# Performance work log

Hardware: AMD Instinct MI355X
Metric: run time of the kernel (lower is better)

## Reference

```python
import jax, jax.numpy as jnp
import numpy as np

H = 16
QK_DIM = 1024
EPS = 1e-5


def setup_inputs() -> dict:
    key = jax.random.key(0)
    ks = jax.random.split(key, 5)
    B, N, M, D = 2, 2048, 2048, 1024
    x = jax.random.normal(ks[0], (B, N, D), jnp.float32)
    context = jax.random.normal(ks[1], (B, M, D), jnp.float32)
    Wq = jax.random.normal(ks[2], (QK_DIM, D), jnp.float32) * (D ** -0.5)
    Wkv = jax.random.normal(ks[3], (QK_DIM + 1024, D), jnp.float32) * (D ** -0.5)
    Wtalk = jax.random.normal(ks[4], (H, H), jnp.float32) * (H ** -0.5)
    ln_gamma = jnp.ones((H,), jnp.float32)
    ln_beta = jnp.zeros((H,), jnp.float32)
    return {"x": x, "context": context, "Wq": Wq, "Wkv": Wkv,
            "Wtalk": Wtalk, "ln_gamma": ln_gamma, "ln_beta": ln_beta}


def _split_heads(t):
    # b n (h d) -> b h n d
    b, n, hd = t.shape
    return t.reshape(b, n, H, hd // H).transpose(0, 2, 1, 3)


def reference(x, context, Wq, Wkv, Wtalk, ln_gamma, ln_beta):
    q = x @ Wq.T                      # [B,N,QK]
    kv = context @ Wkv.T              # [B,M,QK+V]
    k, v = kv[..., :QK_DIM], kv[..., QK_DIM:]
    q, k, v = _split_heads(q), _split_heads(k), _split_heads(v)
    q = q * (q.shape[-1] ** -0.5)
    scores = jnp.einsum('bhid,bhjd->bhij', q, k)          # [B,H,N,M]
    aw = jax.nn.softmax(scores, axis=-1)
    # talking heads: Linear over head axis then LayerNorm over head axis
    aw = jnp.einsum('bhij,gh->bgij', aw, Wtalk)
    mu = jnp.mean(aw, axis=1, keepdims=True)
    var = jnp.var(aw, axis=1, keepdims=True)
    aw = (aw - mu) * jax.lax.rsqrt(var + EPS)
    aw = aw * ln_gamma[None, :, None, None] + ln_beta[None, :, None, None]
    attn = jnp.einsum('bhij,bhjd->bhid', aw, v)           # [B,H,N,dv]
    b, h, n, d = attn.shape
    return attn.transpose(0, 2, 1, 3).reshape(b, n, h * d)  # [B,N,V]
```

## Files before the change

### kernel.cpp

```cpp
#include <hip/hip_runtime.h>


typedef __attribute__((ext_vector_type(8))) short short8;
typedef __attribute__((ext_vector_type(4))) short short4v;
typedef __attribute__((ext_vector_type(4))) float float4v;
typedef unsigned short u16;

#define MFMA16(a, b, c) __builtin_amdgcn_mfma_f32_16x16x32_bf16((a), (b), (c), 0, 0, 0)

__device__ inline u16 f2bf(float f) {
  unsigned u = __float_as_uint(f);
  u += 0x7FFFu + ((u >> 16) & 1u);
  return (u16)(u >> 16);
}

__global__ __launch_bounds__(256) void cast_bf16(const float* __restrict__ in,
                                                 u16* __restrict__ out, int n) {
  int i = (blockIdx.x * 256 + threadIdx.x) * 8;
  if (i + 8 > n) return;
  float4v f0 = *(const float4v*)(in + i);
  float4v f1 = *(const float4v*)(in + i + 4);
  short8 o;
  o[0] = (short)f2bf(f0[0]); o[1] = (short)f2bf(f0[1]);
  o[2] = (short)f2bf(f0[2]); o[3] = (short)f2bf(f0[3]);
  o[4] = (short)f2bf(f1[0]); o[5] = (short)f2bf(f1[1]);
  o[6] = (short)f2bf(f1[2]); o[7] = (short)f2bf(f1[3]);
  *(short8*)(out + i) = o;
}

template <int MODE>
__global__ __launch_bounds__(256, 4) void gemm_bt(const u16* __restrict__ A,
                                                  const u16* __restrict__ W,
                                                  u16* __restrict__ out0,
                                                  u16* __restrict__ out1) {
  __shared__ u16 As[64][40];
  __shared__ u16 Ws[64][40];
  const int t = threadIdx.x;
  const int wave = t >> 6, l = t & 63, l15 = l & 15, lq = l >> 4;
  const int r0 = blockIdx.x * 64, c0 = blockIdx.y * 64;
  const int srow = t >> 2, sch = t & 3;
  const u16* ag = A + (r0 + srow) * 1024 + sch * 8;
  const u16* wg = W + (c0 + srow) * 1024 + sch * 8;

  float4v acc[4];
#pragma unroll
  for (int i = 0; i < 4; ++i) acc[i] = (float4v){0.f, 0.f, 0.f, 0.f};

  short8 av = *(const short8*)ag;
  short8 wv = *(const short8*)wg;
  for (int kt = 0; kt < 32; ++kt) {
    __syncthreads();
    *(short8*)&As[srow][sch * 8] = av;
    *(short8*)&Ws[srow][sch * 8] = wv;
    __syncthreads();
    if (kt < 31) {
      av = *(const short8*)(ag + (kt + 1) * 32);
      wv = *(const short8*)(wg + (kt + 1) * 32);
    }
    short8 af = *(const short8*)&As[wave * 16 + l15][lq * 8];
#pragma unroll
    for (int fn = 0; fn < 4; ++fn) {
      short8 bf = *(const short8*)&Ws[fn * 16 + l15][lq * 8];
      acc[fn] = MFMA16(af, bf, acc[fn]);
    }
  }
#pragma unroll
  for (int fn = 0; fn < 4; ++fn) {
#pragma unroll
    for (int r = 0; r < 4; ++r) {
      int row = r0 + wave * 16 + lq * 4 + r;
      int col = c0 + fn * 16 + l15;
      int b = row >> 11, n = row & 2047;
      float v = acc[fn][r];
      if (MODE == 0) {
        v *= 0.125f;
        int h = col >> 6, d = col & 63;
        out0[(((b * 16 + h) * 2048 + n) << 6) + d] = f2bf(v);
      } else {
        if (col < 1024) {
          int h = col >> 6, d = col & 63;
          out0[(((b * 16 + h) * 2048 + n) << 6) + d] = f2bf(v);
        } else {
          int cc = col - 1024;
          int h = cc >> 6, d = cc & 63;
          out1[(((b * 16 + h) * 2048 + n) << 6) + d] = f2bf(v);
        }
      }
    }
  }
}

__global__ __launch_bounds__(256) void transpose_v(const u16* __restrict__ vh,
                                                   u16* __restrict__ vt) {
  __shared__ u16 tile[64][72];
  const int t = threadIdx.x;
  const int j0 = blockIdx.x * 64, h = blockIdx.y, b = blockIdx.z;
  const u16* src = vh + (((b * 16 + h) * 2048 + j0) << 6);
  int row = t >> 2, c = t & 3;
  short8 v0 = *(const short8*)(src + row * 64 + c * 8);
  short8 v1 = *(const short8*)(src + row * 64 + (c + 4) * 8);
  *(short8*)&tile[row][c * 8] = v0;
  *(short8*)&tile[row][(c + 4) * 8] = v1;
  __syncthreads();
  int d = t >> 2, jc = t & 3;
  short8 o0, o1;
#pragma unroll
  for (int jj = 0; jj < 8; ++jj) o0[jj] = (short)tile[jc * 16 + jj][d];
#pragma unroll
  for (int jj = 0; jj < 8; ++jj) o1[jj] = (short)tile[jc * 16 + 8 + jj][d];
  u16* dst = vt + ((b * 16 + h) * 64 + d) * 2048 + j0 + jc * 16;
  *(short8*)dst = o0;
  *(short8*)(dst + 8) = o1;
}

__global__ __launch_bounds__(1024) void attn_fused(
    const u16* __restrict__ qh, const u16* __restrict__ kh,
    const u16* __restrict__ vt, const float* __restrict__ wtalk,
    const float* __restrict__ gamma, const float* __restrict__ beta,
    float* __restrict__ out) {
  __shared__ u16 P_lds[512 * 36];
  __shared__ u16 Y_lds[16 * 16 * 32];

  const int tid = threadIdx.x;
  const int wv = tid >> 6;
  const int l = tid & 63, l15 = l & 15, lq = l >> 4;
  const int bid = blockIdx.x;
  const int b = bid & 1;
  const int i0 = (bid >> 1) * 16;

  for (int z = tid; z < 512 * 36; z += 1024) P_lds[z] = 0;

  short8 wfrag;
#pragma unroll
  for (int t8 = 0; t8 < 8; ++t8) {
    int h = lq * 8 + t8;
    float wval = (h < 16) ? wtalk[l15 * 16 + h] : 0.f;
    wfrag[t8] = (short)f2bf(wval);
  }
  float gam[4], bet[4];
#pragma unroll
  for (int r = 0; r < 4; ++r) {
    gam[r] = gamma[lq * 4 + r];
    bet[r] = beta[lq * 4 + r];
  }

  const u16* qbase = qh + (((b * 16 + wv) * 2048 + i0) << 6);
  short8 qf0 = *(const short8*)(qbase + l15 * 64 + lq * 8);
  short8 qf1 = *(const short8*)(qbase + l15 * 64 + 32 + lq * 8);
  const u16* kbase = kh + (((b * 16 + wv) * 2048) << 6);
  const u16* vbase = vt + ((b * 16 + wv) * 64) * 2048;

  __syncthreads();

  float ps0 = 0.f, ps1 = 0.f, ps2 = 0.f, ps3 = 0.f;
  short8 k00 = *(const short8*)(kbase + l15 * 64 + lq * 8);
  short8 k01 = *(const short8*)(kbase + l15 * 64 + 32 + lq * 8);
  short8 k10 = *(const short8*)(kbase + (16 + l15) * 64 + lq * 8);
  short8 k11 = *(const short8*)(kbase + (16 + l15) * 64 + 32 + lq * 8);
  for (int jt = 0; jt < 64; ++jt) {
    short8 n00, n01, n10, n11;
    if (jt < 63) {
      const u16* kp = kbase + (((jt + 1) * 32) << 6);
      n00 = *(const short8*)(kp + l15 * 64 + lq * 8);
      n01 = *(const short8*)(kp + l15 * 64 + 32 + lq * 8);
      n10 = *(const short8*)(kp + (16 + l15) * 64 + lq * 8);
      n11 = *(const short8*)(kp + (16 + l15) * 64 + 32 + lq * 8);
    }
    float4v s0 = {0.f, 0.f, 0.f, 0.f}, s1 = {0.f, 0.f, 0.f, 0.f};
    s0 = MFMA16(qf0, k00, s0);
    s0 = MFMA16(qf1, k01, s0);
    s1 = MFMA16(qf0, k10, s1);
    s1 = MFMA16(qf1, k11, s1);
    ps0 += __expf(s0[0]) + __expf(s1[0]);
    ps1 += __expf(s0[1]) + __expf(s1[1]);
    ps2 += __expf(s0[2]) + __expf(s1[2]);
    ps3 += __expf(s0[3]) + __expf(s1[3]);
    k00 = n00; k01 = n01; k10 = n10; k11 = n11;
  }
#pragma unroll
  for (int d = 1; d < 16; d <<= 1) {
    ps0 += __shfl_xor(ps0, d);
    ps1 += __shfl_xor(ps1, d);
    ps2 += __shfl_xor(ps2, d);
    ps3 += __shfl_xor(ps3, d);
  }
  float bc[4];
  bc[0] = -logf(ps0); bc[1] = -logf(ps1);
  bc[2] = -logf(ps2); bc[3] = -logf(ps3);

  float4v acc0 = {0.f, 0.f, 0.f, 0.f}, acc1 = acc0, acc2 = acc0, acc3 = acc0;
  for (int jt = 0; jt < 64; ++jt) {
    const int j0 = jt * 32;
    const u16* kp = kbase + (j0 << 6);
    short8 a00 = *(const short8*)(kp + l15 * 64 + lq * 8);
    short8 a01 = *(const short8*)(kp + l15 * 64 + 32 + lq * 8);
    short8 a10 = *(const short8*)(kp + (16 + l15) * 64 + lq * 8);
    short8 a11 = *(const short8*)(kp + (16 + l15) * 64 + 32 + lq * 8);
    float4v s0 = {0.f, 0.f, 0.f, 0.f}, s1 = {0.f, 0.f, 0.f, 0.f};
    s0 = MFMA16(qf0, a00, s0);
    s0 = MFMA16(qf1, a01, s0);
    s1 = MFMA16(qf0, a10, s1);
    s1 = MFMA16(qf1, a11, s1);
    {
      int ebase = (lq * 4) * 32 + l15;
#pragma unroll
      for (int r = 0; r < 4; ++r) {
        float p0 = __expf(s0[r] + bc[r]);
        float p1 = __expf(s1[r] + bc[r]);
        P_lds[(ebase + r * 32) * 36 + wv] = f2bf(p0);
        P_lds[(ebase + r * 32 + 16) * 36 + wv] = f2bf(p1);
      }
    }
    __syncthreads();
    const u16* vp = vbase + j0 + lq * 8;
    short8 v0 = *(const short8*)(vp + (l15) * 2048);
    short8 v1 = *(const short8*)(vp + (16 + l15) * 2048);
    short8 v2 = *(const short8*)(vp + (32 + l15) * 2048);
    short8 v3 = *(const short8*)(vp + (48 + l15) * 2048);
    float4v t0 = {0.f, 0.f, 0.f, 0.f}, t1 = {0.f, 0.f, 0.f, 0.f};
    {
      int e00 = wv * 32 + l15;
      int e10 = wv * 32 + 16 + l15;
      const u16* p0p = &P_lds[e00 * 36 + lq * 8];
      const u16* p1p = &P_lds[e10 * 36 + lq * 8];
      short4v x0 = *(const short4v*)p0p;
      short4v x1 = *(const short4v*)(p0p + 4);
      short4v y0 = *(const short4v*)p1p;
      short4v y1 = *(const short4v*)(p1p + 4);
      short8 pb0 = __builtin_shufflevector(x0, x1, 0, 1, 2, 3, 4, 5, 6, 7);
      short8 pb1 = __builtin_shufflevector(y0, y1, 0, 1, 2, 3, 4, 5, 6, 7);
      t0 = MFMA16(wfrag, pb0, t0);
      t1 = MFMA16(wfrag, pb1, t1);
    }
#pragma unroll
    for (int c2 = 0; c2 < 2; ++c2) {
      float4v tt = c2 ? t1 : t0;
      float sum = tt[0] + tt[1] + tt[2] + tt[3];
      sum += __shfl_xor(sum, 16);
      sum += __shfl_xor(sum, 32);
      float mu = sum * 0.0625f;
      float ss = tt[0] * tt[0] + tt[1] * tt[1] + tt[2] * tt[2] + tt[3] * tt[3];
      ss += __shfl_xor(ss, 16);
      ss += __shfl_xor(ss, 32);
      float var = ss * 0.0625f - mu * mu;
      float rs = rsqrtf(var + 1e-5f);
#pragma unroll
      for (int r = 0; r < 4; ++r) {
        float y = (tt[r] - mu) * rs * gam[r] + bet[r];
        Y_lds[((lq * 4 + r) * 16 + wv) * 32 + c2 * 16 + l15] = f2bf(y);
      }
    }
    __syncthreads();
    short8 yf = *(const short8*)&Y_lds[(wv * 16 + l15) * 32 + lq * 8];
    acc0 = MFMA16(yf, v0, acc0);
    acc1 = MFMA16(yf, v1, acc1);
    acc2 = MFMA16(yf, v2, acc2);
    acc3 = MFMA16(yf, v3, acc3);
  }
  float* ob = out + (b * 2048 + i0) * 1024 + wv * 64;
#pragma unroll
  for (int r = 0; r < 4; ++r) {
    float* orow = ob + (lq * 4 + r) * 1024;
    orow[l15] = acc0[r];
    orow[16 + l15] = acc1[r];
    orow[32 + l15] = acc2[r];
    orow[48 + l15] = acc3[r];
  }
}

extern "C" void kernel_launch(void* const* d_in, const int* in_sizes, int n_in,
                              void* d_out, int out_size, void* d_ws,
                              size_t ws_size, hipStream_t stream) {
  const float* x = (const float*)d_in[0];
  const float* ctx = (const float*)d_in[1];
  const float* Wq = (const float*)d_in[2];
  const float* Wkv = (const float*)d_in[3];
  const float* Wtalk = (const float*)d_in[4];
  const float* gam = (const float*)d_in[5];
  const float* bet = (const float*)d_in[6];
  float* out = (float*)d_out;

  u16* xb = (u16*)d_ws;
  u16* cb = xb + 4194304;
  u16* wqb = cb + 4194304;
  u16* wkvb = wqb + 1048576;
  u16* qhb = wkvb + 2097152;
  u16* khb = qhb + 4194304;
  u16* vhb = khb + 4194304;
  u16* vtb = vhb + 4194304;

  cast_bf16<<<2048, 256, 0, stream>>>(x, xb, 4194304);
  cast_bf16<<<2048, 256, 0, stream>>>(ctx, cb, 4194304);
  cast_bf16<<<512, 256, 0, stream>>>(Wq, wqb, 1048576);
  cast_bf16<<<1024, 256, 0, stream>>>(Wkv, wkvb, 2097152);

  gemm_bt<0><<<dim3(64, 16), 256, 0, stream>>>(xb, wqb, qhb, nullptr);
  gemm_bt<1><<<dim3(64, 32), 256, 0, stream>>>(cb, wkvb, khb, vhb);

  transpose_v<<<dim3(32, 16, 2), 256, 0, stream>>>(vhb, vtb);

  attn_fused<<<256, 1024, 0, stream>>>(qhb, khb, vtb, Wtalk, gam, bet, out);
}
```

Baseline: 523.4 us.

## Split softmax denominator into separate kernel and split-K attention over key chunks

The softmax log-denominator pass moves out of the fused attention kernel into its own kernel, which writes per-row negative log-sums to workspace. The main attention kernel then splits the key dimension into 8 chunks across a 3D grid and accumulates partial outputs into a zeroed output buffer with atomic adds. This raises block count from 256 to 2048 so the GPU is better occupied, at the cost of a memset, an extra launch, and atomic traffic on the output.

```diff
diff --git a/kernel.cpp b/kernel.cpp
--- a/kernel.cpp
+++ b/kernel.cpp
@@ -113,44 +113,16 @@
   *(short8*)(dst + 8) = o1;
 }
 
-__global__ __launch_bounds__(1024) void attn_fused(
-    const u16* __restrict__ qh, const u16* __restrict__ kh,
-    const u16* __restrict__ vt, const float* __restrict__ wtalk,
-    const float* __restrict__ gamma, const float* __restrict__ beta,
-    float* __restrict__ out) {
-  __shared__ u16 P_lds[512 * 36];
-  __shared__ u16 Y_lds[16 * 16 * 32];
-
-  const int tid = threadIdx.x;
-  const int wv = tid >> 6;
-  const int l = tid & 63, l15 = l & 15, lq = l >> 4;
-  const int bid = blockIdx.x;
-  const int b = bid & 1;
-  const int i0 = (bid >> 1) * 16;
-
-  for (int z = tid; z < 512 * 36; z += 1024) P_lds[z] = 0;
-
-  short8 wfrag;
-#pragma unroll
-  for (int t8 = 0; t8 < 8; ++t8) {
-    int h = lq * 8 + t8;
-    float wval = (h < 16) ? wtalk[l15 * 16 + h] : 0.f;
-    wfrag[t8] = (short)f2bf(wval);
-  }
-  float gam[4], bet[4];
-#pragma unroll
-  for (int r = 0; r < 4; ++r) {
-    gam[r] = gamma[lq * 4 + r];
-    bet[r] = beta[lq * 4 + r];
-  }
-
-  const u16* qbase = qh + (((b * 16 + wv) * 2048 + i0) << 6);
+__global__ __launch_bounds__(256) void denom_kernel(const u16* __restrict__ qh,
+                                                    const u16* __restrict__ kh,
+                                                    float* __restrict__ negl) {
+  const int bh = blockIdx.x;
+  const int i0 = blockIdx.y * 64 + (threadIdx.x >> 6) * 16;
+  const int l = threadIdx.x & 63, l15 = l & 15, lq = l >> 4;
+  const u16* qbase = qh + ((bh * 2048 + i0) << 6);
   short8 qf0 = *(const short8*)(qbase + l15 * 64 + lq * 8);
   short8 qf1 = *(const short8*)(qbase + l15 * 64 + 32 + lq * 8);
-  const u16* kbase = kh + (((b * 16 + wv) * 2048) << 6);
-  const u16* vbase = vt + ((b * 16 + wv) * 64) * 2048;
-
-  __syncthreads();
+  const u16* kbase = kh + ((bh * 2048) << 6);
 
   float ps0 = 0.f, ps1 = 0.f, ps2 = 0.f, ps3 = 0.f;
   short8 k00 = *(const short8*)(kbase + l15 * 64 + lq * 8);
@@ -184,13 +156,59 @@
     ps2 += __shfl_xor(ps2, d);
     ps3 += __shfl_xor(ps3, d);
   }
-  float bc[4];
-  bc[0] = -logf(ps0); bc[1] = -logf(ps1);
-  bc[2] = -logf(ps2); bc[3] = -logf(ps3);
+  if (l15 == 0) {
+    float* o = negl + bh * 2048 + i0 + lq * 4;
+    o[0] = -logf(ps0);
+    o[1] = -logf(ps1);
+    o[2] = -logf(ps2);
+    o[3] = -logf(ps3);
+  }
+}
+
+__global__ __launch_bounds__(1024) void attn_fused(
+    const u16* __restrict__ qh, const u16* __restrict__ kh,
+    const u16* __restrict__ vt, const float* __restrict__ negl,
+    const float* __restrict__ wtalk, const float* __restrict__ gamma,
+    const float* __restrict__ beta, float* __restrict__ out) {
+  __shared__ u16 P_lds[512 * 36];
+  __shared__ u16 Y_lds[16 * 16 * 32];
+
+  const int tid = threadIdx.x;
+  const int wv = tid >> 6;
+  const int l = tid & 63, l15 = l & 15, lq = l >> 4;
+  const int i0 = blockIdx.x * 16;
+  const int jc0 = blockIdx.y * 256;
+  const int b = blockIdx.z;
+  const int bh = b * 16 + wv;
+
+  for (int z = tid; z < 512 * 36; z += 1024) P_lds[z] = 0;
+
+  short8 wfrag;
+#pragma unroll
+  for (int t8 = 0; t8 < 8; ++t8) {
+    int h = lq * 8 + t8;
+    float wval = (h < 16) ? wtalk[l15 * 16 + h] : 0.f;
+    wfrag[t8] = (short)f2bf(wval);
+  }
+  float gam[4], bet[4], bc[4];
+#pragma unroll
+  for (int r = 0; r < 4; ++r) {
+    gam[r] = gamma[lq * 4 + r];
+    bet[r] = beta[lq * 4 + r];
+    bc[r] = negl[bh * 2048 + i0 + lq * 4 + r];
+  }
+
+  const u16* qbase = qh + ((bh * 2048 + i0) << 6);
+  short8 qf0 = *(const short8*)(qbase + l15 * 64 + lq * 8);
+  short8 qf1 = *(const short8*)(qbase + l15 * 64 + 32 + lq * 8);
+  const u16* kbase = kh + ((bh * 2048) << 6);
+  const u16* vbase = vt + (bh * 64) * 2048;
+
+  __syncthreads();
 
   float4v acc0 = {0.f, 0.f, 0.f, 0.f}, acc1 = acc0, acc2 = acc0, acc3 = acc0;
-  for (int jt = 0; jt < 64; ++jt) {
-    const int j0 = jt * 32;
+  for (int jt = 0; jt < 8; ++jt) {
+    const int j0 = jc0 + jt * 32;
     const u16* kp = kbase + (j0 << 6);
     short8 a00 = *(const short8*)(kp + l15 * 64 + lq * 8);
     short8 a01 = *(const short8*)(kp + l15 * 64 + 32 + lq * 8);
@@ -261,10 +279,10 @@
 #pragma unroll
   for (int r = 0; r < 4; ++r) {
     float* orow = ob + (lq * 4 + r) * 1024;
-    orow[l15] = acc0[r];
-    orow[16 + l15] = acc1[r];
-    orow[32 + l15] = acc2[r];
-    orow[48 + l15] = acc3[r];
+    unsafeAtomicAdd(orow + l15, acc0[r]);
+    unsafeAtomicAdd(orow + 16 + l15, acc1[r]);
+    unsafeAtomicAdd(orow + 32 + l15, acc2[r]);
+    unsafeAtomicAdd(orow + 48 + l15, acc3[r]);
   }
 }
 
@@ -288,6 +306,9 @@
   u16* khb = qhb + 4194304;
   u16* vhb = khb + 4194304;
   u16* vtb = vhb + 4194304;
+  float* negl = (float*)(vtb + 4194304);
+
+  hipMemsetAsync(out, 0, 2 * 2048 * 1024 * sizeof(float), stream);
 
   cast_bf16<<<2048, 256, 0, stream>>>(x, xb, 4194304);
   cast_bf16<<<2048, 256, 0, stream>>>(ctx, cb, 4194304);
@@ -299,5 +320,8 @@
 
   transpose_v<<<dim3(32, 16, 2), 256, 0, stream>>>(vhb, vtb);
 
-  attn_fused<<<256, 1024, 0, stream>>>(qhb, khb, vtb, Wtalk, gam, bet, out);
-}
+  denom_kernel<<<dim3(32, 32), 256, 0, stream>>>(qhb, khb, negl);
+
+  attn_fused<<<dim3(128, 8, 2), 1024, 0, stream>>>(qhb, khb, vtb, negl, Wtalk,
+                                                   gam, bet, out);
+}
```

New measurement: 612.4 us. 1.17x slower.

## Double-buffer P and Y tiles to drop one barrier per iteration in attention

Applied to the files above, without the earlier changes.

The attention loop is software-pipelined. P and Y shared-memory tiles are double-buffered, K fragments for the next tile are prefetched, V loads are issued early, and the Y·V MFMA is deferred by one iteration, so each iteration needs one __syncthreads instead of two. Y_lds rows are padded from 32 to 36 to reduce bank conflicts. The grid becomes 2D so that consecutive blocks share the same batch, which may improve cache reuse of K and V. In exchange it doubles LDS use and raises register pressure. The padded 16-byte Y reads are no longer 16-byte aligned, which is a correctness and performance risk.

```diff
diff --git a/kernel.cpp b/kernel.cpp
--- a/kernel.cpp
+++ b/kernel.cpp
@@ -118,17 +118,20 @@
     const u16* __restrict__ vt, const float* __restrict__ wtalk,
     const float* __restrict__ gamma, const float* __restrict__ beta,
     float* __restrict__ out) {
-  __shared__ u16 P_lds[512 * 36];
-  __shared__ u16 Y_lds[16 * 16 * 32];
+  __shared__ u16 P_lds[2][512 * 36];
+  __shared__ u16 Y_lds[2][16 * 16 * 36];
 
   const int tid = threadIdx.x;
   const int wv = tid >> 6;
   const int l = tid & 63, l15 = l & 15, lq = l >> 4;
-  const int bid = blockIdx.x;
-  const int b = bid & 1;
-  const int i0 = (bid >> 1) * 16;
-
-  for (int z = tid; z < 512 * 36; z += 1024) P_lds[z] = 0;
+  const int i0 = blockIdx.x * 16;
+  const int b = blockIdx.y;
+  const int bh = b * 16 + wv;
+
+  {
+    u16* pz = &P_lds[0][0];
+    for (int z = tid; z < 2 * 512 * 36; z += 1024) pz[z] = 0;
+  }
 
   short8 wfrag;
 #pragma unroll
@@ -144,11 +147,11 @@
     bet[r] = beta[lq * 4 + r];
   }
 
-  const u16* qbase = qh + (((b * 16 + wv) * 2048 + i0) << 6);
+  const u16* qbase = qh + ((bh * 2048 + i0) << 6);
   short8 qf0 = *(const short8*)(qbase + l15 * 64 + lq * 8);
   short8 qf1 = *(const short8*)(qbase + l15 * 64 + 32 + lq * 8);
-  const u16* kbase = kh + (((b * 16 + wv) * 2048) << 6);
-  const u16* vbase = vt + ((b * 16 + wv) * 64) * 2048;
+  const u16* kbase = kh + ((bh * 2048) << 6);
+  const u16* vbase = vt + (bh * 64) * 2048;
 
   __syncthreads();
 
@@ -189,73 +192,88 @@
   bc[2] = -logf(ps2); bc[3] = -logf(ps3);
 
   float4v acc0 = {0.f, 0.f, 0.f, 0.f}, acc1 = acc0, acc2 = acc0, acc3 = acc0;
-  for (int jt = 0; jt < 64; ++jt) {
-    const int j0 = jt * 32;
-    const u16* kp = kbase + (j0 << 6);
-    short8 a00 = *(const short8*)(kp + l15 * 64 + lq * 8);
-    short8 a01 = *(const short8*)(kp + l15 * 64 + 32 + lq * 8);
-    short8 a10 = *(const short8*)(kp + (16 + l15) * 64 + lq * 8);
-    short8 a11 = *(const short8*)(kp + (16 + l15) * 64 + 32 + lq * 8);
-    float4v s0 = {0.f, 0.f, 0.f, 0.f}, s1 = {0.f, 0.f, 0.f, 0.f};
-    s0 = MFMA16(qf0, a00, s0);
-    s0 = MFMA16(qf1, a01, s0);
-    s1 = MFMA16(qf0, a10, s1);
-    s1 = MFMA16(qf1, a11, s1);
-    {
+  short8 kc00 = *(const short8*)(kbase + l15 * 64 + lq * 8);
+  short8 kc01 = *(const short8*)(kbase + l15 * 64 + 32 + lq * 8);
+  short8 kc10 = *(const short8*)(kbase + (16 + l15) * 64 + lq * 8);
+  short8 kc11 = *(const short8*)(kbase + (16 + l15) * 64 + 32 + lq * 8);
+  short8 v0, v1, v2, v3;
+
+  for (int jt = 0; jt <= 64; ++jt) {
+    const int buf = jt & 1, pbuf = (jt - 1) & 1;
+    if (jt >= 1) {
+      const u16* vp = vbase + (jt - 1) * 32 + lq * 8;
+      v0 = *(const short8*)(vp + (l15) * 2048);
+      v1 = *(const short8*)(vp + (16 + l15) * 2048);
+      v2 = *(const short8*)(vp + (32 + l15) * 2048);
+      v3 = *(const short8*)(vp + (48 + l15) * 2048);
+    }
+    short8 kn00, kn01, kn10, kn11;
+    if (jt + 1 < 64) {
+      const u16* kp = kbase + (((jt + 1) * 32) << 6);
+      kn00 = *(const short8*)(kp + l15 * 64 + lq * 8);
+      kn01 = *(const short8*)(kp + l15 * 64 + 32 + lq * 8);
+      kn10 = *(const short8*)(kp + (16 + l15) * 64 + lq * 8);
+      kn11 = *(const short8*)(kp + (16 + l15) * 64 + 32 + lq * 8);
+    }
+    if (jt < 64) {
+      float4v s0 = {0.f, 0.f, 0.f, 0.f}, s1 = {0.f, 0.f, 0.f, 0.f};
+      s0 = MFMA16(qf0, kc00, s0);
+      s0 = MFMA16(qf1, kc01, s0);
+      s1 = MFMA16(qf0, kc10, s1);
+      s1 = MFMA16(qf1, kc11, s1);
       int ebase = (lq * 4) * 32 + l15;
 #pragma unroll
       for (int r = 0; r < 4; ++r) {
         float p0 = __expf(s0[r] + bc[r]);
         float p1 = __expf(s1[r] + bc[r]);
-        P_lds[(ebase + r * 32) * 36 + wv] = f2bf(p0);
-        P_lds[(ebase + r * 32 + 16) * 36 + wv] = f2bf(p1);
+        P_lds[buf][(ebase + r * 32) * 36 + wv] = f2bf(p0);
+        P_lds[buf][(ebase + r * 32 + 16) * 36 + wv] = f2bf(p1);
       }
     }
     __syncthreads();
-    const u16* vp = vbase + j0 + lq * 8;
-    short8 v0 = *(const short8*)(vp + (l15) * 2048);
-    short8 v1 = *(const short8*)(vp + (16 + l15) * 2048);
-    short8 v2 = *(const short8*)(vp + (32 + l15) * 2048);
-    short8 v3 = *(const short8*)(vp + (48 + l15) * 2048);
-    float4v t0 = {0.f, 0.f, 0.f, 0.f}, t1 = {0.f, 0.f, 0.f, 0.f};
-    {
-      int e00 = wv * 32 + l15;
-      int e10 = wv * 32 + 16 + l15;
-      const u16* p0p = &P_lds[e00 * 36 + lq * 8];
-      const u16* p1p = &P_lds[e10 * 36 + lq * 8];
-      short4v x0 = *(const short4v*)p0p;
-      short4v x1 = *(const short4v*)(p0p + 4);
-      short4v y0 = *(const short4v*)p1p;
-      short4v y1 = *(const short4v*)(p1p + 4);
-      short8 pb0 = __builtin_shufflevector(x0, x1, 0, 1, 2, 3, 4, 5, 6, 7);
-      short8 pb1 = __builtin_shufflevector(y0, y1, 0, 1, 2, 3, 4, 5, 6, 7);
-      t0 = MFMA16(wfrag, pb0, t0);
-      t1 = MFMA16(wfrag, pb1, t1);
-    }
-#pragma unroll
-    for (int c2 = 0; c2 < 2; ++c2) {
-      float4v tt = c2 ? t1 : t0;
-      float sum = tt[0] + tt[1] + tt[2] + tt[3];
-      sum += __shfl_xor(sum, 16);
-      sum += __shfl_xor(sum, 32);
-      float mu = sum * 0.0625f;
-      float ss = tt[0] * tt[0] + tt[1] * tt[1] + tt[2] * tt[2] + tt[3] * tt[3];
-      ss += __shfl_xor(ss, 16);
-      ss += __shfl_xor(ss, 32);
-      float var = ss * 0.0625f - mu * mu;
-      float rs = rsqrtf(var + 1e-5f);
-#pragma unroll
-      for (int r = 0; r < 4; ++r) {
-        float y = (tt[r] - mu) * rs * gam[r] + bet[r];
-        Y_lds[((lq * 4 + r) * 16 + wv) * 32 + c2 * 16 + l15] = f2bf(y);
+    if (jt < 64) {
+      float4v t0 = {0.f, 0.f, 0.f, 0.f}, t1 = {0.f, 0.f, 0.f, 0.f};
+      {
+        int e00 = wv * 32 + l15;
+        int e10 = wv * 32 + 16 + l15;
+        const u16* p0p = &P_lds[buf][e00 * 36 + lq * 8];
+        const u16* p1p = &P_lds[buf][e10 * 36 + lq * 8];
+        short4v x0 = *(const short4v*)p0p;
+        short4v x1 = *(const short4v*)(p0p + 4);
+        short4v y0 = *(const short4v*)p1p;
+        short4v y1 = *(const short4v*)(p1p + 4);
+        short8 pb0 = __builtin_shufflevector(x0, x1, 0, 1, 2, 3, 4, 5, 6, 7);
+        short8 pb1 = __builtin_shufflevector(y0, y1, 0, 1, 2, 3, 4, 5, 6, 7);
+        t0 = MFMA16(wfrag, pb0, t0);
+        t1 = MFMA16(wfrag, pb1, t1);
       }
-    }
-    __syncthreads();
-    short8 yf = *(const short8*)&Y_lds[(wv * 16 + l15) * 32 + lq * 8];
-    acc0 = MFMA16(yf, v0, acc0);
-    acc1 = MFMA16(yf, v1, acc1);
-    acc2 = MFMA16(yf, v2, acc2);
-    acc3 = MFMA16(yf, v3, acc3);
+#pragma unroll
+      for (int c2 = 0; c2 < 2; ++c2) {
+        float4v tt = c2 ? t1 : t0;
+        float sum = tt[0] + tt[1] + tt[2] + tt[3];
+        sum += __shfl_xor(sum, 16);
+        sum += __shfl_xor(sum, 32);
+        float mu = sum * 0.0625f;
+        float ss = tt[0] * tt[0] + tt[1] * tt[1] + tt[2] * tt[2] + tt[3] * tt[3];
+        ss += __shfl_xor(ss, 16);
+        ss += __shfl_xor(ss, 32);
+        float var = ss * 0.0625f - mu * mu;
+        float rs = rsqrtf(var + 1e-5f);
+#pragma unroll
+        for (int r = 0; r < 4; ++r) {
+          float y = (tt[r] - mu) * rs * gam[r] + bet[r];
+          Y_lds[buf][((lq * 4 + r) * 16 + wv) * 36 + c2 * 16 + l15] = f2bf(y);
+        }
+      }
+    }
+    if (jt >= 1) {
+      short8 yf = *(const short8*)&Y_lds[pbuf][(wv * 16 + l15) * 36 + lq * 8];
+      acc0 = MFMA16(yf, v0, acc0);
+      acc1 = MFMA16(yf, v1, acc1);
+      acc2 = MFMA16(yf, v2, acc2);
+      acc3 = MFMA16(yf, v3, acc3);
+    }
+    kc00 = kn00; kc01 = kn01; kc10 = kn10; kc11 = kn11;
   }
   float* ob = out + (b * 2048 + i0) * 1024 + wv * 64;
 #pragma unroll
@@ -299,5 +317,6 @@
 
   transpose_v<<<dim3(32, 16, 2), 256, 0, stream>>>(vhb, vtb);
 
-  attn_fused<<<256, 1024, 0, stream>>>(qhb, khb, vtb, Wtalk, gam, bet, out);
-}
+  attn_fused<<<dim3(128, 2), 1024, 0, stream>>>(qhb, khb, vtb, Wtalk, gam, bet,
+                                                out);
+}
```

After: 506.7 us. -3.2%, faster.

## Split attention into denominator and split-key PV kernels with atomic accumulation

Applied to the files above, without the earlier changes.

Replaces the single fused attention kernel, which ran 256 blocks of 1024 threads, with two kernels. A separate denominator kernel computes the softmax sums over key chunks and accumulates them with atomics. A split-key PV kernel then runs 1024 blocks of 256 threads, where each wave handles 4 heads, and atomically adds partial outputs into a zeroed output buffer. The aim is more parallelism and better occupancy across CUs. The cost is extra memsets, float atomics on the full output, and a second pass recomputing QK scores.

```diff
diff --git a/kernel.cpp b/kernel.cpp
--- a/kernel.cpp
+++ b/kernel.cpp
@@ -5,6 +5,7 @@
 typedef __attribute__((ext_vector_type(4))) short short4v;
 typedef __attribute__((ext_vector_type(4))) float float4v;
 typedef unsigned short u16;
+typedef unsigned int u32;
 
 #define MFMA16(a, b, c) __builtin_amdgcn_mfma_f32_16x16x32_bf16((a), (b), (c), 0, 0, 0)
 
@@ -113,53 +114,27 @@
   *(short8*)(dst + 8) = o1;
 }
 
-__global__ __launch_bounds__(1024) void attn_fused(
-    const u16* __restrict__ qh, const u16* __restrict__ kh,
-    const u16* __restrict__ vt, const float* __restrict__ wtalk,
-    const float* __restrict__ gamma, const float* __restrict__ beta,
-    float* __restrict__ out) {
-  __shared__ u16 P_lds[512 * 36];
-  __shared__ u16 Y_lds[16 * 16 * 32];
-
-  const int tid = threadIdx.x;
-  const int wv = tid >> 6;
-  const int l = tid & 63, l15 = l & 15, lq = l >> 4;
+__global__ __launch_bounds__(256) void denom_kernel(const u16* __restrict__ qh,
+                                                    const u16* __restrict__ kh,
+                                                    float* __restrict__ lsum) {
   const int bid = blockIdx.x;
-  const int b = bid & 1;
-  const int i0 = (bid >> 1) * 16;
-
-  for (int z = tid; z < 512 * 36; z += 1024) P_lds[z] = 0;
-
-  short8 wfrag;
-#pragma unroll
-  for (int t8 = 0; t8 < 8; ++t8) {
-    int h = lq * 8 + t8;
-    float wval = (h < 16) ? wtalk[l15 * 16 + h] : 0.f;
-    wfrag[t8] = (short)f2bf(wval);
-  }
-  float gam[4], bet[4];
-#pragma unroll
-  for (int r = 0; r < 4; ++r) {
-    gam[r] = gamma[lq * 4 + r];
-    bet[r] = beta[lq * 4 + r];
-  }
-
-  const u16* qbase = qh + (((b * 16 + wv) * 2048 + i0) << 6);
+  const int bh = bid & 31, it = (bid >> 5) & 31, jc = bid >> 10;
+  const int wv = threadIdx.x >> 6;
+  const int i0 = it * 64 + wv * 16;
+  const int l = threadIdx.x & 63, l15 = l & 15, lq = l >> 4;
+  const u16* qbase = qh + ((bh * 2048 + i0) << 6);
   short8 qf0 = *(const short8*)(qbase + l15 * 64 + lq * 8);
   short8 qf1 = *(const short8*)(qbase + l15 * 64 + 32 + lq * 8);
-  const u16* kbase = kh + (((b * 16 + wv) * 2048) << 6);
-  const u16* vbase = vt + ((b * 16 + wv) * 64) * 2048;
-
-  __syncthreads();
+  const u16* kbase = kh + ((bh * 2048 + jc * 512) << 6);
 
   float ps0 = 0.f, ps1 = 0.f, ps2 = 0.f, ps3 = 0.f;
   short8 k00 = *(const short8*)(kbase + l15 * 64 + lq * 8);
   short8 k01 = *(const short8*)(kbase + l15 * 64 + 32 + lq * 8);
   short8 k10 = *(const short8*)(kbase + (16 + l15) * 64 + lq * 8);
   short8 k11 = *(const short8*)(kbase + (16 + l15) * 64 + 32 + lq * 8);
-  for (int jt = 0; jt < 64; ++jt) {
+  for (int jt = 0; jt < 16; ++jt) {
     short8 n00, n01, n10, n11;
-    if (jt < 63) {
+    if (jt < 15) {
       const u16* kp = kbase + (((jt + 1) * 32) << 6);
       n00 = *(const short8*)(kp + l15 * 64 + lq * 8);
       n01 = *(const short8*)(kp + l15 * 64 + 32 + lq * 8);
@@ -184,88 +159,139 @@
     ps2 += __shfl_xor(ps2, d);
     ps3 += __shfl_xor(ps3, d);
   }
-  float bc[4];
-  bc[0] = -logf(ps0); bc[1] = -logf(ps1);
-  bc[2] = -logf(ps2); bc[3] = -logf(ps3);
-
-  float4v acc0 = {0.f, 0.f, 0.f, 0.f}, acc1 = acc0, acc2 = acc0, acc3 = acc0;
-  for (int jt = 0; jt < 64; ++jt) {
-    const int j0 = jt * 32;
-    const u16* kp = kbase + (j0 << 6);
-    short8 a00 = *(const short8*)(kp + l15 * 64 + lq * 8);
-    short8 a01 = *(const short8*)(kp + l15 * 64 + 32 + lq * 8);
-    short8 a10 = *(const short8*)(kp + (16 + l15) * 64 + lq * 8);
-    short8 a11 = *(const short8*)(kp + (16 + l15) * 64 + 32 + lq * 8);
-    float4v s0 = {0.f, 0.f, 0.f, 0.f}, s1 = {0.f, 0.f, 0.f, 0.f};
-    s0 = MFMA16(qf0, a00, s0);
-    s0 = MFMA16(qf1, a01, s0);
-    s1 = MFMA16(qf0, a10, s1);
-    s1 = MFMA16(qf1, a11, s1);
-    {
-      int ebase = (lq * 4) * 32 + l15;
+  if (l15 == 0) {
+    const int b = bh >> 4, h = bh & 15;
+    float* o = lsum + ((b * 2048) + i0 + lq * 4) * 16 + h;
+    unsafeAtomicAdd(o, ps0);
+    unsafeAtomicAdd(o + 16, ps1);
+    unsafeAtomicAdd(o + 32, ps2);
+    unsafeAtomicAdd(o + 48, ps3);
+  }
+}
+
+__global__ __launch_bounds__(256) void attn_pv(
+    const u16* __restrict__ qh, const u16* __restrict__ kh,
+    const u16* __restrict__ vt, const float* __restrict__ lsum,
+    const float* __restrict__ wtalk, const float* __restrict__ gamma,
+    const float* __restrict__ beta, float* __restrict__ out) {
+  __shared__ u16 P_lds[512 * 36];
+  __shared__ u16 Y_lds[16 * 16 * 36];
+
+  const int tid = threadIdx.x;
+  const int wv = tid >> 6, l = tid & 63, l15 = l & 15, lq = l >> 4;
+  const int slot = blockIdx.x & 7;
+  const int jc = slot >> 1, b = slot & 1;
+  const int it = blockIdx.x >> 3;
+  const int i0 = it * 16, jbase = jc * 512;
+  const int hbase = wv * 4;
+
+  for (int z = tid; z < 512 * 36; z += 256) P_lds[z] = 0;
+
+  short8 wfrag;
+#pragma unroll
+  for (int t8 = 0; t8 < 8; ++t8) {
+    int h = lq * 8 + t8;
+    wfrag[t8] = (h < 16) ? (short)f2bf(wtalk[l15 * 16 + h]) : (short)0;
+  }
+  float gam[4], bet[4];
+#pragma unroll
+  for (int r = 0; r < 4; ++r) {
+    gam[r] = gamma[lq * 4 + r];
+    bet[r] = beta[lq * 4 + r];
+  }
+  float rl[4][4];
+#pragma unroll
+  for (int hh = 0; hh < 4; ++hh)
+#pragma unroll
+    for (int r = 0; r < 4; ++r)
+      rl[hh][r] =
+          1.0f / lsum[((b * 2048) + i0 + lq * 4 + r) * 16 + hbase + hh];
+  short8 qf[4][2];
+#pragma unroll
+  for (int hh = 0; hh < 4; ++hh) {
+    const u16* qp =
+        qh + (((b * 16 + hbase + hh) * 2048 + i0 + l15) << 6) + lq * 8;
+    qf[hh][0] = *(const short8*)qp;
+    qf[hh][1] = *(const short8*)(qp + 32);
+  }
+
+  float4v acc[4][4];
+#pragma unroll
+  for (int gg = 0; gg < 4; ++gg)
+#pragma unroll
+    for (int dd = 0; dd < 4; ++dd) acc[gg][dd] = (float4v){0.f, 0.f, 0.f, 0.f};
+
+  __syncthreads();
+
+  for (int sj = 0; sj < 16; ++sj) {
+    const int j0 = jbase + sj * 32;
+#pragma unroll
+    for (int hh = 0; hh < 4; ++hh) {
+      const int h = hbase + hh;
+      const u16* kp = kh + (((b * 16 + h) * 2048 + j0) << 6);
+      short8 k00 = *(const short8*)(kp + l15 * 64 + lq * 8);
+      short8 k01 = *(const short8*)(kp + l15 * 64 + 32 + lq * 8);
+      short8 k10 = *(const short8*)(kp + (16 + l15) * 64 + lq * 8);
+      short8 k11 = *(const short8*)(kp + (16 + l15) * 64 + 32 + lq * 8);
+      float4v s0 = {0.f, 0.f, 0.f, 0.f}, s1 = {0.f, 0.f, 0.f, 0.f};
+      s0 = MFMA16(qf[hh][0], k00, s0);
+      s0 = MFMA16(qf[hh][1], k01, s0);
+      s1 = MFMA16(qf[hh][0], k10, s1);
+      s1 = MFMA16(qf[hh][1], k11, s1);
 #pragma unroll
       for (int r = 0; r < 4; ++r) {
-        float p0 = __expf(s0[r] + bc[r]);
-        float p1 = __expf(s1[r] + bc[r]);
-        P_lds[(ebase + r * 32) * 36 + wv] = f2bf(p0);
-        P_lds[(ebase + r * 32 + 16) * 36 + wv] = f2bf(p1);
+        const int e0 = (lq * 4 + r) * 32 + l15;
+        P_lds[e0 * 36 + h] = f2bf(__expf(s0[r]) * rl[hh][r]);
+        P_lds[(e0 + 16) * 36 + h] = f2bf(__expf(s1[r]) * rl[hh][r]);
       }
     }
     __syncthreads();
-    const u16* vp = vbase + j0 + lq * 8;
-    short8 v0 = *(const short8*)(vp + (l15) * 2048);
-    short8 v1 = *(const short8*)(vp + (16 + l15) * 2048);
-    short8 v2 = *(const short8*)(vp + (32 + l15) * 2048);
-    short8 v3 = *(const short8*)(vp + (48 + l15) * 2048);
-    float4v t0 = {0.f, 0.f, 0.f, 0.f}, t1 = {0.f, 0.f, 0.f, 0.f};
-    {
-      int e00 = wv * 32 + l15;
-      int e10 = wv * 32 + 16 + l15;
-      const u16* p0p = &P_lds[e00 * 36 + lq * 8];
-      const u16* p1p = &P_lds[e10 * 36 + lq * 8];
-      short4v x0 = *(const short4v*)p0p;
-      short4v x1 = *(const short4v*)(p0p + 4);
-      short4v y0 = *(const short4v*)p1p;
-      short4v y1 = *(const short4v*)(p1p + 4);
-      short8 pb0 = __builtin_shufflevector(x0, x1, 0, 1, 2, 3, 4, 5, 6, 7);
-      short8 pb1 = __builtin_shufflevector(y0, y1, 0, 1, 2, 3, 4, 5, 6, 7);
-      t0 = MFMA16(wfrag, pb0, t0);
-      t1 = MFMA16(wfrag, pb1, t1);
-    }
-#pragma unroll
-    for (int c2 = 0; c2 < 2; ++c2) {
-      float4v tt = c2 ? t1 : t0;
-      float sum = tt[0] + tt[1] + tt[2] + tt[3];
+#pragma unroll
+    for (int c = 0; c < 8; ++c) {
+      const int e = wv * 128 + c * 16 + l15;
+      const u16* pp = &P_lds[e * 36 + lq * 8];
+      short4v x0 = *(const short4v*)pp;
+      short4v x1 = *(const short4v*)(pp + 4);
+      short8 pb = __builtin_shufflevector(x0, x1, 0, 1, 2, 3, 4, 5, 6, 7);
+      float4v t = MFMA16(wfrag, pb, ((float4v){0.f, 0.f, 0.f, 0.f}));
+      float sum = t[0] + t[1] + t[2] + t[3];
       sum += __shfl_xor(sum, 16);
       sum += __shfl_xor(sum, 32);
       float mu = sum * 0.0625f;
-      float ss = tt[0] * tt[0] + tt[1] * tt[1] + tt[2] * tt[2] + tt[3] * tt[3];
+      float ss = t[0] * t[0] + t[1] * t[1] + t[2] * t[2] + t[3] * t[3];
       ss += __shfl_xor(ss, 16);
       ss += __shfl_xor(ss, 32);
       float var = ss * 0.0625f - mu * mu;
       float rs = rsqrtf(var + 1e-5f);
+      const int ii = e >> 5, jl = e & 31;
 #pragma unroll
       for (int r = 0; r < 4; ++r) {
-        float y = (tt[r] - mu) * rs * gam[r] + bet[r];
-        Y_lds[((lq * 4 + r) * 16 + wv) * 32 + c2 * 16 + l15] = f2bf(y);
+        float y = (t[r] - mu) * rs * gam[r] + bet[r];
+        Y_lds[((lq * 4 + r) * 16 + ii) * 36 + jl] = f2bf(y);
       }
     }
     __syncthreads();
-    short8 yf = *(const short8*)&Y_lds[(wv * 16 + l15) * 32 + lq * 8];
-    acc0 = MFMA16(yf, v0, acc0);
-    acc1 = MFMA16(yf, v1, acc1);
-    acc2 = MFMA16(yf, v2, acc2);
-    acc3 = MFMA16(yf, v3, acc3);
-  }
-  float* ob = out + (b * 2048 + i0) * 1024 + wv * 64;
-#pragma unroll
-  for (int r = 0; r < 4; ++r) {
-    float* orow = ob + (lq * 4 + r) * 1024;
-    orow[l15] = acc0[r];
-    orow[16 + l15] = acc1[r];
-    orow[32 + l15] = acc2[r];
-    orow[48 + l15] = acc3[r];
-  }
+#pragma unroll
+    for (int gg = 0; gg < 4; ++gg) {
+      const int g = hbase + gg;
+      short8 yf = *(const short8*)&Y_lds[(g * 16 + l15) * 36 + lq * 8];
+      const u16* vb = vt + ((size_t)(b * 16 + g) * 64) * 2048 + j0 + lq * 8;
+#pragma unroll
+      for (int dd = 0; dd < 4; ++dd) {
+        short8 vf = *(const short8*)(vb + (dd * 16 + l15) * 2048);
+        acc[gg][dd] = MFMA16(yf, vf, acc[gg][dd]);
+      }
+    }
+  }
+#pragma unroll
+  for (int gg = 0; gg < 4; ++gg)
+#pragma unroll
+    for (int dd = 0; dd < 4; ++dd)
+#pragma unroll
+      for (int r = 0; r < 4; ++r)
+        unsafeAtomicAdd(out + (size_t)((b * 2048) + i0 + lq * 4 + r) * 1024 +
+                            (hbase + gg) * 64 + dd * 16 + l15,
+                        acc[gg][dd][r]);
 }
 
 extern "C" void kernel_launch(void* const* d_in, const int* in_sizes, int n_in,
@@ -288,6 +314,10 @@
   u16* khb = qhb + 4194304;
   u16* vhb = khb + 4194304;
   u16* vtb = vhb + 4194304;
+  float* lsum = (float*)(vtb + 4194304);
+
+  hipMemsetAsync(lsum, 0, 262144, stream);
+  hipMemsetAsync(out, 0, (size_t)2 * 2048 * 1024 * sizeof(float), stream);
 
   cast_bf16<<<2048, 256, 0, stream>>>(x, xb, 4194304);
   cast_bf16<<<2048, 256, 0, stream>>>(ctx, cb, 4194304);
@@ -299,5 +329,7 @@
 
   transpose_v<<<dim3(32, 16, 2), 256, 0, stream>>>(vhb, vtb);
 
-  attn_fused<<<256, 1024, 0, stream>>>(qhb, khb, vtb, Wtalk, gam, bet, out);
-}
+  denom_kernel<<<4096, 256, 0, stream>>>(qhb, khb, lsum);
+
+  attn_pv<<<1024, 256, 0, stream>>>(qhb, khb, vtb, lsum, Wtalk, gam, bet, out);
+}
```

Measured after the change: 688.7 us. 31.6% more time.
